# Kernel optimization log

Hardware: AMD Instinct MI355X
Metric: run time of the kernel (lower is better)

## Reference

```python
import jax, jax.numpy as jnp
import numpy as np

ORDER = 2            # spline order kx = ky
H = W = 7            # control_grid_dims
KSZ = 3.0            # kernel_size -> bbox = (-1.5, 1.5)
OUT, IN = 32, 32     # out_channels, in_groups (groups=1)
N = 32768            # number of query points
BBOX = KSZ / 2.0


def _make_knots(n_coef, lo, hi, order):
    # clamped knot vector of length n_coef + order + 1 (as scipy produces)
    n_interior = n_coef - order - 1
    interior = np.linspace(lo, hi, n_interior + 2)[1:-1]
    t = np.concatenate([[lo] * (order + 1), interior, [hi] * (order + 1)])
    return jnp.asarray(t, dtype=jnp.float32)


def setup_inputs() -> dict:
    key = jax.random.key(0)
    k1, k2 = jax.random.split(key)
    # query points strictly inside the bbox
    xy = jax.random.uniform(k1, (N, 2), dtype=jnp.float32,
                            minval=-BBOX * 0.95, maxval=BBOX * 0.95)
    # control coefficients C: [out_channels, in_groups, h, w]
    C = jax.random.normal(k2, (OUT, IN, H, W), dtype=jnp.float32) * 0.1
    Tx = _make_knots(H, -BBOX, BBOX, ORDER)
    Ty = _make_knots(W, -BBOX, BBOX, ORDER)
    return {"xy": xy, "Tx": Tx, "Ty": Ty, "C": C}


def _find_span(T, v, p):
    # torch: (T <= v).min(dim=-1) -> first False index, minus 1; if all True -> len(T)-p-2
    ss = jnp.searchsorted(T, v, side="right")          # number of knots <= v
    return jnp.where(ss == T.shape[0], T.shape[0] - p - 2, ss - 1)


def _safe_div(num, den):
    return num / jnp.where(den == 0, jnp.ones_like(den), den)


def reference(xy, Tx, Ty, C):
    px = py = ORDER
    X = xy[:, 0]
    Y = xy[:, 1]
    kx = _find_span(Tx, X, px)   # [N] knot spans
    ky = _find_span(Ty, Y, py)

    dim = OUT * IN
    Ctrl = C.reshape(dim, H, W)
    offs = jnp.arange(px + 1)
    ix = kx[:, None] - px + offs                 # [N, px+1]
    iy = ky[:, None] - py + offs                 # [N, py+1]
    # gather local (px+1)x(py+1) control patch per point: [N, Dim, px+1, py+1]
    D = Ctrl[:, ix[:, :, None], iy[:, None, :]]
    D = jnp.transpose(D, (1, 0, 2, 3))

    rng = jnp.arange(px)
    # de Boor recursion along x
    for r in range(1, px + 1):
        t_lo = Tx[kx[:, None] - px + 1 + rng]    # [N, px]
        t_hi = Tx[kx[:, None] + 2 - r + rng]
        alphax = _safe_div(X[:, None] - t_lo, t_hi - t_lo)
        for j in range(px, r - 1, -1):
            a = alphax[:, j - 1][:, None, None]
            D = D.at[:, :, j, :].set((1 - a) * D[:, :, j - 1, :] + a * D[:, :, j, :])
    # de Boor recursion along y (on the collapsed x row px)
    for r in range(1, py + 1):
        t_lo = Ty[ky[:, None] - py + 1 + rng]
        t_hi = Ty[ky[:, None] + 2 - r + rng]
        alphay = _safe_div(Y[:, None] - t_lo, t_hi - t_lo)
        for j in range(py, r - 1, -1):
            a = alphay[:, j - 1][:, None]
            D = D.at[:, :, px, j].set((1 - a) * D[:, :, px, j - 1] + a * D[:, :, px, j])

    return D[:, :, px, py].reshape(xy.shape[0], OUT, IN)
```

## Files before the change

kernel.cpp:

```cpp
#include <hip/hip_runtime.h>


#define NPTS   32768
#define DIM    1024
#define MT     (NPTS / 16)
#define WELEM  (MT * 2 * 64 * 8)

typedef _Float16 f16x8 __attribute__((ext_vector_type(8)));
typedef float    f32x4 __attribute__((ext_vector_type(4)));

__device__ __forceinline__ float safe_div(float n, float d) {
    return (d == 0.0f) ? n : (n / d);
}

__device__ __forceinline__ void span_weights(float v, const float* __restrict__ T,
                                             int& k, float& w0, float& w1, float& w2) {
    float t3 = T[3], t4 = T[4], t5 = T[5], t6 = T[6];
    k = 2 + (v >= t3) + (v >= t4) + (v >= t5) + (v >= t6);
    float Tm1 = T[k - 1], T0 = T[k], Tp1 = T[k + 1], Tp2 = T[k + 2];
    float a10 = safe_div(v - Tm1, Tp1 - Tm1);
    float a11 = safe_div(v - T0,  Tp2 - T0);
    float a21 = safe_div(v - T0,  Tp1 - T0);
    w0 = (1.0f - a21) * (1.0f - a10);
    w1 = (1.0f - a21) * a10 + a21 * (1.0f - a11);
    w2 = a21 * a11;
}

__global__ __launch_bounds__(256) void prep_kernel(
    const float* __restrict__ xy,
    const float* __restrict__ Tx,
    const float* __restrict__ Ty,
    const float* __restrict__ C,
    _Float16* __restrict__ Wp,
    _Float16* __restrict__ Cp)
{
    const int b = blockIdx.x;
    const int t = threadIdx.x;
    if (b < MT / 2) {
        const int id   = b * 256 + t;
        const int lane = id & 63;
        const int step = (id >> 6) & 1;
        const int tile = id >> 7;
        const int n    = tile * 16 + (lane & 15);
        const int g    = lane >> 4;

        const float2 pt = ((const float2*)xy)[n];
        int kx, ky;
        float wx0, wx1, wx2, wy0, wy1, wy2;
        span_weights(pt.x, Tx, kx, wx0, wx1, wx2);
        span_weights(pt.y, Ty, ky, wy0, wy1, wy2);
        const int off = (kx - 2) * 7 + (ky - 2);

        f16x8 frag;
#pragma unroll
        for (int j = 0; j < 8; ++j) {
            const int k   = step * 32 + g * 8 + j;
            const int rel = k - off;
            const float va = (rel >= 14) ? wx2 : ((rel >= 7) ? wx1 : wx0);
            const int   bb = rel - ((rel >= 14) ? 14 : ((rel >= 7) ? 7 : 0));
            const float vb = (bb == 0) ? wy0 : ((bb == 1) ? wy1 : wy2);
            const bool valid = (rel >= 0) && (rel <= 16) && (bb >= 0) && (bb <= 2);
            frag[j] = (_Float16)(valid ? va * vb : 0.0f);
        }
        *(f16x8*)(Wp + (size_t)id * 8) = frag;
    } else if (b < MT / 2 + 32) {
        const int id    = (b - MT / 2) * 256 + t;
        const int lane  = id & 63;
        const int step  = (id >> 6) & 1;
        const int ctile = id >> 7;
        const int ch    = ctile * 16 + (lane & 15);
        const int g     = lane >> 4;

        f16x8 frag;
#pragma unroll
        for (int j = 0; j < 8; ++j) {
            const int k = step * 32 + g * 8 + j;
            frag[j] = (_Float16)((k < 49) ? C[(size_t)ch * 49 + k] : 0.0f);
        }
        *(f16x8*)(Cp + (size_t)id * 8) = frag;
    }
}

__global__ __launch_bounds__(256, 4) void spline_mfma_kernel(
    const _Float16* __restrict__ Wp,
    const _Float16* __restrict__ Cp,
    float* __restrict__ out)
{
    __shared__ float lds[4 * 1024];

    const int t      = threadIdx.x;
    const int lane   = t & 63;
    const int w      = t >> 6;
    const int chgrp  = blockIdx.x & 3;
    const int pchunk = blockIdx.x >> 2;

    float* const wbuf = lds + w * 1024;

    f16x8 af[4][2];
#pragma unroll
    for (int ct = 0; ct < 4; ++ct)
#pragma unroll
        for (int st = 0; st < 2; ++st) {
            const int ctg = chgrp * 16 + w * 4 + ct;
            af[ct][st] = *(const f16x8*)(Cp + ((size_t)(ctg * 2 + st) * 64 + lane) * 8);
        }

    const int p = lane & 15;
    const int h = lane >> 4;
    const int cb = lane & 15;

    const int ptile0 = pchunk * 8;
    f16x8 nb0 = *(const f16x8*)(Wp + ((size_t)(ptile0 * 2 + 0) * 64 + lane) * 8);
    f16x8 nb1 = *(const f16x8*)(Wp + ((size_t)(ptile0 * 2 + 1) * 64 + lane) * 8);

#pragma unroll
    for (int pt = 0; pt < 8; ++pt) {
        const int ptile = pchunk * 8 + pt;
        const f16x8 b0 = nb0;
        const f16x8 b1 = nb1;
        if (pt + 1 < 8) {
            nb0 = *(const f16x8*)(Wp + ((size_t)((ptile + 1) * 2 + 0) * 64 + lane) * 8);
            nb1 = *(const f16x8*)(Wp + ((size_t)((ptile + 1) * 2 + 1) * 64 + lane) * 8);
        }

        f32x4 acc[4];
#pragma unroll
        for (int ct = 0; ct < 4; ++ct) {
            f32x4 z; z[0] = 0.0f; z[1] = 0.0f; z[2] = 0.0f; z[3] = 0.0f;
            acc[ct] = __builtin_amdgcn_mfma_f32_16x16x32_f16(af[ct][0], b0, z, 0, 0, 0);
        }
#pragma unroll
        for (int ct = 0; ct < 4; ++ct)
            acc[ct] = __builtin_amdgcn_mfma_f32_16x16x32_f16(af[ct][1], b1, acc[ct], 0, 0, 0);

#pragma unroll
        for (int ct = 0; ct < 4; ++ct) {
            const int g16 = ct * 4 + h;
            const int col = (g16 & 8) | ((g16 ^ p) & 7);
            *(f32x4*)(wbuf + p * 64 + (col << 2)) = acc[ct];
        }

#pragma unroll
        for (int gg = 0; gg < 4; ++gg) {
            const int pr  = gg * 4 + h;
            const int col = (cb & 8) | ((cb ^ pr) & 7);
            f32x4 v = *(const f32x4*)(wbuf + pr * 64 + (col << 2));
            float* dst = out + (size_t)(ptile * 16 + pr) * DIM
                             + chgrp * 256 + w * 64 + cb * 4;
            *(f32x4*)dst = v;
        }
    }
}

extern "C" void kernel_launch(void* const* d_in, const int* in_sizes, int n_in,
                              void* d_out, int out_size, void* d_ws, size_t ws_size,
                              hipStream_t stream) {
    const float* xy = (const float*)d_in[0];
    const float* Tx = (const float*)d_in[1];
    const float* Ty = (const float*)d_in[2];
    const float* C  = (const float*)d_in[3];
    float* out = (float*)d_out;

    _Float16* Wp = (_Float16*)d_ws;
    _Float16* Cp = Wp + WELEM;

    prep_kernel<<<MT / 2 + 32, 256, 0, stream>>>(xy, Tx, Ty, C, Wp, Cp);
    spline_mfma_kernel<<<4 * (MT / 8), 256, 0, stream>>>(Wp, Cp, out);
}
```

Measured before the change: 38.20 us.

## Fuse weight and coefficient packing into the MFMA kernel via LDS

Drops the separate prep kernel. Each block now computes the fp16 spline-weight fragments for its 128 points into shared memory and converts its slice of C to fp16 fragments in registers directly. This removes one launch and the global workspace round-trip for the packed weights and coefficients. In exchange, the weight math is repeated in each of the 4 channel-group blocks, C is read with strided scalar loads, and a block-wide barrier is added before the MFMA loop.

```diff
diff --git a/kernel.cpp b/kernel.cpp
--- a/kernel.cpp
+++ b/kernel.cpp
@@ -3,8 +3,6 @@
 
 #define NPTS   32768
 #define DIM    1024
-#define MT     (NPTS / 16)
-#define WELEM  (MT * 2 * 64 * 8)
 
 typedef _Float16 f16x8 __attribute__((ext_vector_type(8)));
 typedef float    f32x4 __attribute__((ext_vector_type(4)));
@@ -26,67 +24,15 @@
     w2 = a21 * a11;
 }
 
-__global__ __launch_bounds__(256) void prep_kernel(
+__global__ __launch_bounds__(256, 4) void spline_fused_kernel(
+    const float* __restrict__ C,
     const float* __restrict__ xy,
     const float* __restrict__ Tx,
     const float* __restrict__ Ty,
-    const float* __restrict__ C,
-    _Float16* __restrict__ Wp,
-    _Float16* __restrict__ Cp)
-{
-    const int b = blockIdx.x;
-    const int t = threadIdx.x;
-    if (b < MT / 2) {
-        const int id   = b * 256 + t;
-        const int lane = id & 63;
-        const int step = (id >> 6) & 1;
-        const int tile = id >> 7;
-        const int n    = tile * 16 + (lane & 15);
-        const int g    = lane >> 4;
-
-        const float2 pt = ((const float2*)xy)[n];
-        int kx, ky;
-        float wx0, wx1, wx2, wy0, wy1, wy2;
-        span_weights(pt.x, Tx, kx, wx0, wx1, wx2);
-        span_weights(pt.y, Ty, ky, wy0, wy1, wy2);
-        const int off = (kx - 2) * 7 + (ky - 2);
-
-        f16x8 frag;
-#pragma unroll
-        for (int j = 0; j < 8; ++j) {
-            const int k   = step * 32 + g * 8 + j;
-            const int rel = k - off;
-            const float va = (rel >= 14) ? wx2 : ((rel >= 7) ? wx1 : wx0);
-            const int   bb = rel - ((rel >= 14) ? 14 : ((rel >= 7) ? 7 : 0));
-            const float vb = (bb == 0) ? wy0 : ((bb == 1) ? wy1 : wy2);
-            const bool valid = (rel >= 0) && (rel <= 16) && (bb >= 0) && (bb <= 2);
-            frag[j] = (_Float16)(valid ? va * vb : 0.0f);
-        }
-        *(f16x8*)(Wp + (size_t)id * 8) = frag;
-    } else if (b < MT / 2 + 32) {
-        const int id    = (b - MT / 2) * 256 + t;
-        const int lane  = id & 63;
-        const int step  = (id >> 6) & 1;
-        const int ctile = id >> 7;
-        const int ch    = ctile * 16 + (lane & 15);
-        const int g     = lane >> 4;
-
-        f16x8 frag;
-#pragma unroll
-        for (int j = 0; j < 8; ++j) {
-            const int k = step * 32 + g * 8 + j;
-            frag[j] = (_Float16)((k < 49) ? C[(size_t)ch * 49 + k] : 0.0f);
-        }
-        *(f16x8*)(Cp + (size_t)id * 8) = frag;
-    }
-}
-
-__global__ __launch_bounds__(256, 4) void spline_mfma_kernel(
-    const _Float16* __restrict__ Wp,
-    const _Float16* __restrict__ Cp,
     float* __restrict__ out)
 {
-    __shared__ float lds[4 * 1024];
+    __shared__ _Float16 wrec[8][128][8];
+    __shared__ float    tbuf[4][1024];
 
     const int t      = threadIdx.x;
     const int lane   = t & 63;
@@ -94,34 +40,65 @@
     const int chgrp  = blockIdx.x & 3;
     const int pchunk = blockIdx.x >> 2;
 
-    float* const wbuf = lds + w * 1024;
+    if (t < 128) {
+        const int p = pchunk * 128 + t;
+        const float2 pt2 = ((const float2*)xy)[p];
+        int kx, ky;
+        float wx0, wx1, wx2, wy0, wy1, wy2;
+        span_weights(pt2.x, Tx, kx, wx0, wx1, wx2);
+        span_weights(pt2.y, Ty, ky, wy0, wy1, wy2);
+        const int off = (kx - 2) * 7 + (ky - 2);
+#pragma unroll
+        for (int c = 0; c < 8; ++c) {
+            f16x8 frag;
+#pragma unroll
+            for (int j = 0; j < 8; ++j) {
+                const int k   = 32 * (c >> 2) + 8 * (c & 3) + j;
+                const int rel = k - off;
+                const float va = (rel >= 14) ? wx2 : ((rel >= 7) ? wx1 : wx0);
+                const int   bb = rel - ((rel >= 14) ? 14 : ((rel >= 7) ? 7 : 0));
+                const float vb = (bb == 0) ? wy0 : ((bb == 1) ? wy1 : wy2);
+                const bool valid = (rel >= 0) && (rel <= 16) && (bb >= 0) && (bb <= 2);
+                frag[j] = (_Float16)(valid ? va * vb : 0.0f);
+            }
+            *(f16x8*)&wrec[c][t][0] = frag;
+        }
+    }
 
     f16x8 af[4][2];
+    {
+        const int colch = lane & 15;
+        const int g     = lane >> 4;
 #pragma unroll
-    for (int ct = 0; ct < 4; ++ct)
+        for (int ct = 0; ct < 4; ++ct) {
+            const int ch = (chgrp * 16 + w * 4 + ct) * 16 + colch;
+            const float* crow = C + (size_t)ch * 49;
 #pragma unroll
-        for (int st = 0; st < 2; ++st) {
-            const int ctg = chgrp * 16 + w * 4 + ct;
-            af[ct][st] = *(const f16x8*)(Cp + ((size_t)(ctg * 2 + st) * 64 + lane) * 8);
+            for (int st = 0; st < 2; ++st) {
+                f16x8 frag;
+#pragma unroll
+                for (int j = 0; j < 8; ++j) {
+                    const int k = st * 32 + g * 8 + j;
+                    frag[j] = (_Float16)((k < 49) ? crow[k] : 0.0f);
+                }
+                af[ct][st] = frag;
+            }
         }
+    }
 
-    const int p = lane & 15;
-    const int h = lane >> 4;
+    __syncthreads();
+
+    const int p  = lane & 15;
+    const int h  = lane >> 4;
     const int cb = lane & 15;
-
-    const int ptile0 = pchunk * 8;
-    f16x8 nb0 = *(const f16x8*)(Wp + ((size_t)(ptile0 * 2 + 0) * 64 + lane) * 8);
-    f16x8 nb1 = *(const f16x8*)(Wp + ((size_t)(ptile0 * 2 + 1) * 64 + lane) * 8);
+    float* const wbuf = &tbuf[w][0];
 
 #pragma unroll
     for (int pt = 0; pt < 8; ++pt) {
         const int ptile = pchunk * 8 + pt;
-        const f16x8 b0 = nb0;
-        const f16x8 b1 = nb1;
-        if (pt + 1 < 8) {
-            nb0 = *(const f16x8*)(Wp + ((size_t)((ptile + 1) * 2 + 0) * 64 + lane) * 8);
-            nb1 = *(const f16x8*)(Wp + ((size_t)((ptile + 1) * 2 + 1) * 64 + lane) * 8);
-        }
+
+        const f16x8 b0 = *(const f16x8*)&wrec[h][pt * 16 + p][0];
+        const f16x8 b1 = *(const f16x8*)&wrec[4 + h][pt * 16 + p][0];
 
         f32x4 acc[4];
 #pragma unroll
@@ -161,9 +138,5 @@
     const float* C  = (const float*)d_in[3];
     float* out = (float*)d_out;
 
-    _Float16* Wp = (_Float16*)d_ws;
-    _Float16* Cp = Wp + WELEM;
-
-    prep_kernel<<<MT / 2 + 32, 256, 0, stream>>>(xy, Tx, Ty, C, Wp, Cp);
-    spline_mfma_kernel<<<4 * (MT / 8), 256, 0, stream>>>(Wp, Cp, out);
+    spline_fused_kernel<<<4 * (NPTS / 128), 256, 0, stream>>>(C, xy, Tx, Ty, out);
 }
```

Measured after the change: 40.06 us. 4.9% more time.
